# Performance work log

Hardware: AMD Instinct MI355X
Metric: run time of the kernel (lower is better)

## Reference

```python
import jax, jax.numpy as jnp
import numpy as np

WPB = [4, 2, 2]          # words_per_block per scale
NH = 8                   # num_heads
DIM = 256                # feature dim (uniform, required by cross-scale einsums)
HD = DIM // NH           # per-head feature dim
W_PAR, W_PEER, W_KID = 0.5, 1.0, 2.0


def _linear(x, W):
    # torch nn.Linear (no bias): W is [out, in]
    return jnp.einsum('bhwi,oi->bhwo', x, W)


def _split_heads(y):
    # 'b h w (k f) -> b k h w f'
    b, H, Wd, D = y.shape
    return jnp.transpose(y.reshape(b, H, Wd, NH, D // NH), (0, 3, 1, 2, 4))


def _query(x, W):
    return _split_heads(_linear(x, W))


def _kv(x, W):
    # 'b h w (i k f) -> i b k h w f' with i=2
    y = _linear(x, W)
    b, H, Wd, D = y.shape
    y = y.reshape(b, H, Wd, 2, NH, D // (2 * NH))
    y = jnp.transpose(y, (3, 0, 4, 1, 2, 5))
    return y[0], y[1]


def _blocks(x, hb):
    # 'b k (h1 h2) (w1 w2) f -> b k h1 w1 (h2 w2) f'
    b, k, H, Wd, f = x.shape
    h1, w1 = H // hb, Wd // hb
    x = x.reshape(b, k, h1, hb, w1, hb, f)
    return jnp.transpose(x, (0, 1, 2, 4, 3, 5, 6)).reshape(b, k, h1, w1, hb * hb, f)


def _forward(xs, qpeer, kvpeer, qpar, kvpar, qkid, kvkid):
    n = len(WPB)
    outs = []
    for i in range(n):
        hb = WPB[i]
        hk = WPB[i + 1] if i < n - 1 else 0
        npar = 1 if i > 0 else 0
        scale = (hb + npar + hk) ** -0.5  # coupled scaling (decouple_scales=False)
        x = xs[i]
        b, Hi, Wi, _ = x.shape
        h1, w1 = Hi // hb, Wi // hb
        L = hb * hb  # queries per block
        attn, val, wts = [], [], []
        # --- peers ---
        qp = _blocks(_query(x, qpeer[i]), hb)
        kp, vp = _kv(x, kvpeer[i])
        kp, vp = _blocks(kp, hb), _blocks(vp, hb)
        attn.append(jnp.einsum('bkhwlf,bkhwmf->bkhwlm', qp, kp) * scale)
        val.append(jnp.broadcast_to(vp[:, :, :, :, None], (b, NH, h1, w1, L, L, HD)))
        wts.append(W_PEER * jnp.ones((L,), jnp.float32))
        # --- parents ---
        if i > 0:
            qpa = _blocks(_query(x, qpar[i - 1]), hb)
            kpa, vpa = _kv(xs[i - 1], kvpar[i - 1])  # [b,k,h1,w1,f]
            attn.append(jnp.einsum('bkhwlf,bkhwf->bkhwl', qpa, kpa)[..., None] * scale)
            val.append(jnp.broadcast_to(vpa[:, :, :, :, None, None, :], (b, NH, h1, w1, L, 1, HD)))
            wts.append(W_PAR * jnp.ones((1,), jnp.float32))
        # --- kids ---
        if i < n - 1:
            g = hk * hk
            qk = _query(x, qkid[i])               # [b,k,Hi,Wi,f]
            kk, vk = _kv(xs[i + 1], kvkid[i])
            kkb = _blocks(kk, hk)                  # [b,k,Hi,Wi,g,f]
            a = jnp.einsum('bkhwf,bkhwgf->bkhwg', qk, kkb) * scale
            a = jnp.transpose(a.reshape(b, NH, h1, hb, w1, hb, g), (0, 1, 2, 4, 3, 5, 6)).reshape(b, NH, h1, w1, L, g)
            attn.append(a)
            vkb = vk.reshape(b, NH, h1, hb, hk, w1, hb, hk, HD)
            vkb = jnp.transpose(vkb, (0, 1, 2, 5, 3, 6, 4, 7, 8)).reshape(b, NH, h1, w1, L, g, HD)
            val.append(vkb)
            wts.append(W_KID * jnp.ones((g,), jnp.float32))
        V = jnp.concatenate(val, axis=-2)          # [b,k,h1,w1,L,M,f]
        wvec = jnp.concatenate(wts)                # [M]
        A = jax.nn.softmax(jnp.concatenate(attn, axis=-1), axis=-1)
        A = wvec * A
        A = A / A.sum(-1, keepdims=True)
        # NOTE: faithful to the source einsum 'bkhwlm,bkhwlnf->bkhwlf' where m and n
        # are independently summed indices (attn row-sum times value sum over n).
        o = jnp.einsum('bkhwlm,bkhwlnf->bkhwlf', A, V)
        # 'b k h1 w1 (h2 w2) f -> b (h1 h2) (w1 w2) (k f)'
        o = jnp.transpose(o.reshape(b, NH, h1, w1, hb, hb, HD), (0, 2, 4, 3, 5, 1, 6)).reshape(b, Hi, Wi, NH * HD)
        outs.append(o)
    # forward returns ms_proj_drop(ms_slf_attn): projection output is discarded in the
    # source (ms_out is overwritten), and dropout is identity at p=0.
    return tuple(outs)


def setup_inputs() -> dict:
    key = jax.random.key(0)
    ks = iter(jax.random.split(key, 24))
    B = 8
    Hs = [16, 32, 64]
    d = {}
    for i in range(3):
        d[f'x{i}'] = jax.random.normal(next(ks), (B, Hs[i], Hs[i], DIM), jnp.float32)
    for i in range(3):
        d[f'qpeer_w{i}'] = 0.02 * jax.random.normal(next(ks), (DIM, DIM), jnp.float32)
        d[f'kvpeer_w{i}'] = 0.02 * jax.random.normal(next(ks), (2 * DIM, DIM), jnp.float32)
    for i in (1, 2):
        d[f'qpar_w{i}'] = 0.02 * jax.random.normal(next(ks), (DIM, DIM), jnp.float32)
        d[f'kvpar_w{i}'] = 0.02 * jax.random.normal(next(ks), (2 * DIM, DIM), jnp.float32)
    for i in (0, 1):
        d[f'qkid_w{i}'] = 0.02 * jax.random.normal(next(ks), (DIM, DIM), jnp.float32)
        d[f'kvkid_w{i}'] = 0.02 * jax.random.normal(next(ks), (2 * DIM, DIM), jnp.float32)
    return d


def reference(x0, x1, x2, qpeer_w0, qpeer_w1, qpeer_w2, kvpeer_w0, kvpeer_w1, kvpeer_w2,
              qpar_w1, qpar_w2, kvpar_w1, kvpar_w2, qkid_w0, qkid_w1, kvkid_w0, kvkid_w1):
    return _forward([x0, x1, x2],
                    [qpeer_w0, qpeer_w1, qpeer_w2],
                    [kvpeer_w0, kvpeer_w1, kvpeer_w2],
                    [qpar_w1, qpar_w2],
                    [kvpar_w1, kvpar_w2],
                    [qkid_w0, qkid_w1],
                    [kvkid_w0, kvkid_w1])
```

## Files before the change

### kernel.cpp

```cpp
#include <hip/hip_runtime.h>


constexpr int FD = 256;

typedef __attribute__((ext_vector_type(8))) short short8;
typedef __attribute__((ext_vector_type(4))) float floatx4;

__device__ inline unsigned short bf16bits(float f) {
  unsigned u = __builtin_bit_cast(unsigned, f);
  return (unsigned short)((u + 0x7fffu + ((u >> 16) & 1u)) >> 16);
}

__device__ inline short8 load_cvt8(const float* p) {
  float4 a = *(const float4*)p;
  float4 b = *(const float4*)(p + 4);
  short8 r;
  r[0] = (short)bf16bits(a.x); r[1] = (short)bf16bits(a.y);
  r[2] = (short)bf16bits(a.z); r[3] = (short)bf16bits(a.w);
  r[4] = (short)bf16bits(b.x); r[5] = (short)bf16bits(b.y);
  r[6] = (short)bf16bits(b.z); r[7] = (short)bf16bits(b.w);
  return r;
}

constexpr size_t OFF_S1 = 144 * 256;
constexpr size_t OFF_S2 = OFF_S1 + 2048 * 256;
constexpr size_t OFF_W = OFF_S2 + 8192 * 256;

__global__ __launch_bounds__(256) void prep(
    const float4* __restrict__ x0, const float4* __restrict__ x1,
    const float4* __restrict__ x2, const float* __restrict__ wp0,
    const float* __restrict__ wk0, const float* __restrict__ wp1,
    const float* __restrict__ wq1, const float* __restrict__ wk1,
    const float* __restrict__ wp2, const float* __restrict__ wq2,
    unsigned short* __restrict__ ws) {
  int blk = blockIdx.x;
  int t = threadIdx.x;
  if (blk < 2592) {
    const float4* x;
    unsigned short* S;
    int Hs, Ws, hb, row0;
    if (blk < 32) {
      x = x0; S = ws; Hs = 4; Ws = 4; hb = 4; row0 = blk * 4;
    } else if (blk < 544) {
      x = x1; S = ws + OFF_S1; Hs = 16; Ws = 16; hb = 2; row0 = (blk - 32) * 4;
    } else {
      x = x2; S = ws + OFF_S2; Hs = 32; Ws = 32; hb = 2; row0 = (blk - 544) * 4;
    }
    int c = t & 63;
    int row = row0 + (t >> 6);
    int bw = row % Ws;
    int t2 = row / Ws;
    int bh = t2 % Hs;
    int b = t2 / Hs;
    int W = Ws * hb;
    const float4* xb =
        x + (((size_t)b * Hs * hb + bh * hb) * W + bw * hb) * 64 + c;
    float4 s = {0.f, 0.f, 0.f, 0.f};
    for (int i = 0; i < hb; ++i)
      for (int j = 0; j < hb; ++j) {
        float4 v = xb[((size_t)i * W + j) * 64];
        s.x += v.x; s.y += v.y; s.z += v.z; s.w += v.w;
      }
    ushort4 o = {bf16bits(s.x), bf16bits(s.y), bf16bits(s.z), bf16bits(s.w)};
    *(ushort4*)(S + (size_t)row * FD + c * 4) = o;
  } else {
    int wb = blk - 2592;
    int mat = wb >> 6;
    int row = (wb & 63) * 4 + (t >> 6);
    int c4 = (t & 63) * 4;
    const float* src;
    switch (mat) {
      case 0: src = wp0; break;
      case 1: src = wk0; break;
      case 2: src = wp1; break;
      case 3: src = wq1; break;
      case 4: src = wk1; break;
      case 5: src = wp2; break;
      default: src = wq2; break;
    }
    float4 v = *(const float4*)(src + (size_t)(256 + row) * FD + c4);
    ushort4 o = {bf16bits(v.x), bf16bits(v.y), bf16bits(v.z), bf16bits(v.w)};
    *(ushort4*)(ws + OFF_W + (size_t)mat * 65536 + (size_t)row * FD + c4) = o;
  }
}

#define MFMA(a, b, c) __builtin_amdgcn_mfma_f32_16x16x32_bf16(a, b, c, 0, 0, 0)

__global__ __launch_bounds__(256) void gemm12(
    const unsigned short* __restrict__ ws, const float* __restrict__ x0,
    float* __restrict__ out0, float* __restrict__ out1) {
  bool segB = blockIdx.x >= 128;
  int bid = segB ? blockIdx.x - 128 : blockIdx.x;
  int r0 = (bid >> 2) * 64;
  int n0 = (bid & 3) * 64;
  int l = threadIdx.x & 63;
  int wv = threadIdx.x >> 6;
  int c = l & 15, q = l >> 4;
  int n = n0 + wv * 16 + c;
  const short8* S1b = (const short8*)(ws + OFF_S1);
  const short8* Wb = (const short8*)(ws + OFF_W);
  const short8* aS[4];
#pragma unroll
  for (int mt = 0; mt < 4; ++mt)
    aS[mt] = S1b + (size_t)(r0 + mt * 16 + c) * 32 + q;

  if (!segB) {
    const short8* aC = (const short8*)ws + (size_t)((r0 >> 4) + c) * 32 + q;
    const short8* bK = Wb + (size_t)1 * 8192 + n * 32 + q;
    const short8* bP = Wb + (size_t)0 * 8192 + n * 32 + q;
    floatx4 accK[4] = {0, 0, 0, 0};
    floatx4 accC = {0, 0, 0, 0};
#pragma unroll 2
    for (int kk = 0; kk < 8; ++kk) {
      short8 b0 = bK[kk * 4];
      short8 b1 = bP[kk * 4];
#pragma unroll
      for (int mt = 0; mt < 4; ++mt) accK[mt] = MFMA(aS[mt][kk * 4], b0, accK[mt]);
      accC = MFMA(aC[kk * 4], b1, accC);
    }
    float s0 = __shfl(accC[0], c), s1 = __shfl(accC[1], c);
    float s2 = __shfl(accC[2], c), s3 = __shfl(accC[3], c);
    float cv = q == 0 ? s0 : q == 1 ? s1 : q == 2 ? s2 : s3;
#pragma unroll
    for (int mt = 0; mt < 4; ++mt)
#pragma unroll
      for (int r = 0; r < 4; ++r) {
        int row = r0 + mt * 16 + 4 * q + r;
        out0[(size_t)row * FD + n] = accK[mt][r] + cv;
      }
  } else {
    const float* aX[4];
#pragma unroll
    for (int mt = 0; mt < 4; ++mt)
      aX[mt] = x0 + (size_t)(r0 + mt * 16 + c) * FD + q * 8;
    const short8* bP = Wb + (size_t)2 * 8192 + n * 32 + q;
    const short8* bQ = Wb + (size_t)3 * 8192 + n * 32 + q;
    floatx4 acc[4] = {0, 0, 0, 0};
#pragma unroll 2
    for (int kk = 0; kk < 8; ++kk) {
      short8 b0 = bP[kk * 4];
      short8 b1 = bQ[kk * 4];
#pragma unroll
      for (int mt = 0; mt < 4; ++mt) {
        acc[mt] = MFMA(aS[mt][kk * 4], b0, acc[mt]);
        acc[mt] = MFMA(load_cvt8(aX[mt] + kk * 32), b1, acc[mt]);
      }
    }
#pragma unroll
    for (int mt = 0; mt < 4; ++mt)
#pragma unroll
      for (int r = 0; r < 4; ++r) {
        int rg = r0 + mt * 16 + 4 * q + r;
        int b = rg >> 8, h = (rg >> 4) & 15, w = rg & 15;
        size_t o = ((size_t)b * 1024 + h * 64 + 2 * w) * FD + n;
        float v = acc[mt][r];
        out1[o] = v;
        out1[o + FD] = v;
        out1[o + 8192] = v;
        out1[o + 8192 + FD] = v;
      }
  }
}

__global__ __launch_bounds__(256) void gemm3(
    const unsigned short* __restrict__ ws, const float* __restrict__ x1,
    float* __restrict__ out1, float* __restrict__ out2) {
  int r0 = (blockIdx.x >> 2) * 64;
  int n0 = (blockIdx.x & 3) * 64;
  int l = threadIdx.x & 63;
  int wv = threadIdx.x >> 6;
  int c = l & 15, q = l >> 4;
  int n = n0 + wv * 16 + c;
  const short8* S2b = (const short8*)(ws + OFF_S2);
  const short8* Wb = (const short8*)(ws + OFF_W);
  const short8* aS[4];
  const float* aX[4];
#pragma unroll
  for (int mt = 0; mt < 4; ++mt) {
    aS[mt] = S2b + (size_t)(r0 + mt * 16 + c) * 32 + q;
    aX[mt] = x1 + (size_t)(r0 + mt * 16 + c) * FD + q * 8;
  }
  const short8* bK = Wb + (size_t)4 * 8192 + n * 32 + q;
  const short8* bP = Wb + (size_t)5 * 8192 + n * 32 + q;
  const short8* bQ = Wb + (size_t)6 * 8192 + n * 32 + q;
  floatx4 accK[4] = {0, 0, 0, 0};
  floatx4 accC[4] = {0, 0, 0, 0};
#pragma unroll 2
  for (int kk = 0; kk < 8; ++kk) {
    short8 b0 = bK[kk * 4];
    short8 b1 = bP[kk * 4];
    short8 b2 = bQ[kk * 4];
#pragma unroll
    for (int mt = 0; mt < 4; ++mt) {
      short8 a = aS[mt][kk * 4];
      accK[mt] = MFMA(a, b0, accK[mt]);
      accC[mt] = MFMA(a, b1, accC[mt]);
      accC[mt] = MFMA(load_cvt8(aX[mt] + kk * 32), b2, accC[mt]);
    }
  }
#pragma unroll
  for (int mt = 0; mt < 4; ++mt)
#pragma unroll
    for (int r = 0; r < 4; ++r) {
      int rg = r0 + mt * 16 + 4 * q + r;
      size_t o1 = (size_t)rg * FD + n;
      out1[o1] += accK[mt][r];
      int b = rg >> 10, h = (rg >> 5) & 31, w = rg & 31;
      size_t o = ((size_t)b * 4096 + h * 128 + 2 * w) * FD + n;
      float v = accC[mt][r];
      out2[o] = v;
      out2[o + FD] = v;
      out2[o + 16384] = v;
      out2[o + 16384 + FD] = v;
    }
}

extern "C" void kernel_launch(void* const* d_in, const int* in_sizes, int n_in,
                              void* d_out, int out_size, void* d_ws,
                              size_t ws_size, hipStream_t stream) {
  const float* x0 = (const float*)d_in[0];
  const float* x1 = (const float*)d_in[1];
  const float* x2 = (const float*)d_in[2];

  const float *kvpeer0, *kvpeer1, *kvpeer2, *kvpar1, *kvpar2, *kvkid0, *kvkid1;
  if (n_in > 4 && in_sizes[4] == 2 * FD * FD) {
    kvpeer0 = (const float*)d_in[4];
    kvpeer1 = (const float*)d_in[6];
    kvpeer2 = (const float*)d_in[8];
    kvpar1 = (const float*)d_in[10];
    kvpar2 = (const float*)d_in[12];
    kvkid0 = (const float*)d_in[14];
    kvkid1 = (const float*)d_in[16];
  } else {
    kvpeer0 = (const float*)d_in[6];
    kvpeer1 = (const float*)d_in[7];
    kvpeer2 = (const float*)d_in[8];
    kvpar1 = (const float*)d_in[11];
    kvpar2 = (const float*)d_in[12];
    kvkid0 = (const float*)d_in[15];
    kvkid1 = (const float*)d_in[16];
  }

  unsigned short* ws = (unsigned short*)d_ws;
  float* out0 = (float*)d_out;
  float* out1 = out0 + (size_t)8 * 16 * 16 * FD;
  float* out2 = out1 + (size_t)8 * 32 * 32 * FD;

  prep<<<3040, 256, 0, stream>>>((const float4*)x0, (const float4*)x1,
                                 (const float4*)x2, kvpeer0, kvkid0, kvpeer1,
                                 kvpar1, kvkid1, kvpeer2, kvpar2, ws);
  gemm12<<<256, 256, 0, stream>>>(ws, x0, out0, out1);
  gemm3<<<512, 256, 0, stream>>>(ws, x1, out1, out2);
}
```

Measured before the change: 174.5 us.

## Merge gemm12 and gemm3 into one launch, pre-converting x0/x1 to bf16 in prep

The prep kernel now also writes bf16 copies of x0 and x1 to workspace while it sums blocks, so the GEMMs no longer convert fp32 activations inside their inner loops. The two GEMM kernels are merged into one 640-block launch. Each out1 tile now computes the parent contribution itself and adds it to the kid term through LDS, instead of gemm3 doing a read-modify-write of out1 after gemm12. This removes a launch, a kernel boundary and an extra out1 pass, at the cost of more workspace traffic in prep and some redundant parent-term MFMAs in each block.

```diff
diff --git a/kernel.cpp b/kernel.cpp
--- a/kernel.cpp
+++ b/kernel.cpp
@@ -10,21 +10,18 @@
   unsigned u = __builtin_bit_cast(unsigned, f);
   return (unsigned short)((u + 0x7fffu + ((u >> 16) & 1u)) >> 16);
 }
-
-__device__ inline short8 load_cvt8(const float* p) {
-  float4 a = *(const float4*)p;
-  float4 b = *(const float4*)(p + 4);
-  short8 r;
-  r[0] = (short)bf16bits(a.x); r[1] = (short)bf16bits(a.y);
-  r[2] = (short)bf16bits(a.z); r[3] = (short)bf16bits(a.w);
-  r[4] = (short)bf16bits(b.x); r[5] = (short)bf16bits(b.y);
-  r[6] = (short)bf16bits(b.z); r[7] = (short)bf16bits(b.w);
-  return r;
+__device__ inline ushort4 cvt4(float4 v) {
+  ushort4 o;
+  o.x = bf16bits(v.x); o.y = bf16bits(v.y);
+  o.z = bf16bits(v.z); o.w = bf16bits(v.w);
+  return o;
 }
 
 constexpr size_t OFF_S1 = 144 * 256;
 constexpr size_t OFF_S2 = OFF_S1 + 2048 * 256;
 constexpr size_t OFF_W = OFF_S2 + 8192 * 256;
+constexpr size_t OFF_X0 = OFF_W + 7 * 65536;
+constexpr size_t OFF_X1 = OFF_X0 + 2048 * 256;
 
 __global__ __launch_bounds__(256) void prep(
     const float4* __restrict__ x0, const float4* __restrict__ x1,
@@ -38,11 +35,13 @@
   if (blk < 2592) {
     const float4* x;
     unsigned short* S;
+    unsigned short* xo = nullptr;
     int Hs, Ws, hb, row0;
     if (blk < 32) {
-      x = x0; S = ws; Hs = 4; Ws = 4; hb = 4; row0 = blk * 4;
+      x = x0; S = ws; xo = ws + OFF_X0; Hs = 4; Ws = 4; hb = 4; row0 = blk * 4;
     } else if (blk < 544) {
-      x = x1; S = ws + OFF_S1; Hs = 16; Ws = 16; hb = 2; row0 = (blk - 32) * 4;
+      x = x1; S = ws + OFF_S1; xo = ws + OFF_X1;
+      Hs = 16; Ws = 16; hb = 2; row0 = (blk - 32) * 4;
     } else {
       x = x2; S = ws + OFF_S2; Hs = 32; Ws = 32; hb = 2; row0 = (blk - 544) * 4;
     }
@@ -53,16 +52,16 @@
     int bh = t2 % Hs;
     int b = t2 / Hs;
     int W = Ws * hb;
-    const float4* xb =
-        x + (((size_t)b * Hs * hb + bh * hb) * W + bw * hb) * 64 + c;
+    size_t base4 = (((size_t)b * Hs * hb + bh * hb) * W + bw * hb) * 64 + c;
+    const float4* xb = x + base4;
     float4 s = {0.f, 0.f, 0.f, 0.f};
     for (int i = 0; i < hb; ++i)
       for (int j = 0; j < hb; ++j) {
-        float4 v = xb[((size_t)i * W + j) * 64];
+        float4 v = xb[(size_t)(i * W + j) * 64];
         s.x += v.x; s.y += v.y; s.z += v.z; s.w += v.w;
+        if (xo) *(ushort4*)(xo + (base4 + (size_t)(i * W + j) * 64) * 4) = cvt4(v);
       }
-    ushort4 o = {bf16bits(s.x), bf16bits(s.y), bf16bits(s.z), bf16bits(s.w)};
-    *(ushort4*)(S + (size_t)row * FD + c * 4) = o;
+    *(ushort4*)(S + (size_t)row * FD + c * 4) = cvt4(s);
   } else {
     int wb = blk - 2592;
     int mat = wb >> 6;
@@ -79,44 +78,100 @@
       default: src = wq2; break;
     }
     float4 v = *(const float4*)(src + (size_t)(256 + row) * FD + c4);
-    ushort4 o = {bf16bits(v.x), bf16bits(v.y), bf16bits(v.z), bf16bits(v.w)};
-    *(ushort4*)(ws + OFF_W + (size_t)mat * 65536 + (size_t)row * FD + c4) = o;
+    *(ushort4*)(ws + OFF_W + (size_t)mat * 65536 + (size_t)row * FD + c4) =
+        cvt4(v);
   }
 }
 
 #define MFMA(a, b, c) __builtin_amdgcn_mfma_f32_16x16x32_bf16(a, b, c, 0, 0, 0)
 
-__global__ __launch_bounds__(256) void gemm12(
-    const unsigned short* __restrict__ ws, const float* __restrict__ x0,
-    float* __restrict__ out0, float* __restrict__ out1) {
-  bool segB = blockIdx.x >= 128;
-  int bid = segB ? blockIdx.x - 128 : blockIdx.x;
-  int r0 = (bid >> 2) * 64;
-  int n0 = (bid & 3) * 64;
-  int l = threadIdx.x & 63;
-  int wv = threadIdx.x >> 6;
+__global__ __launch_bounds__(256) void gemm(const unsigned short* __restrict__ ws,
+                                            float* __restrict__ out0,
+                                            float* __restrict__ out1,
+                                            float* __restrict__ out2) {
+  __shared__ float lds[4][16][17];
+  int t = threadIdx.x;
+  int l = t & 63;
+  int wv = t >> 6;
   int c = l & 15, q = l >> 4;
-  int n = n0 + wv * 16 + c;
-  const short8* S1b = (const short8*)(ws + OFF_S1);
   const short8* Wb = (const short8*)(ws + OFF_W);
-  const short8* aS[4];
-#pragma unroll
-  for (int mt = 0; mt < 4; ++mt)
-    aS[mt] = S1b + (size_t)(r0 + mt * 16 + c) * 32 + q;
-
-  if (!segB) {
+
+  if (blockIdx.x < 512) {
+    int r0 = (blockIdx.x >> 2) * 64;
+    int n0 = (blockIdx.x & 3) * 64;
+    int n = n0 + wv * 16 + c;
+    const short8* S2b = (const short8*)(ws + OFF_S2);
+    const short8* X1b = (const short8*)(ws + OFF_X1);
+    int cb0 = (r0 >> 10) * 256 + (((r0 >> 5) & 31) >> 1) * 16;
+    const short8* aS1 = (const short8*)(ws + OFF_S1) + (size_t)(cb0 + c) * 32 + q;
+    const short8* aX0 = (const short8*)(ws + OFF_X0) + (size_t)(cb0 + c) * 32 + q;
+    const short8 *aS2[4], *aX1[4];
+#pragma unroll
+    for (int mt = 0; mt < 4; ++mt) {
+      aS2[mt] = S2b + (size_t)(r0 + mt * 16 + c) * 32 + q;
+      aX1[mt] = X1b + (size_t)(r0 + mt * 16 + c) * 32 + q;
+    }
+    const short8* bK1 = Wb + (size_t)4 * 8192 + (size_t)n * 32 + q;
+    const short8* bP2 = Wb + (size_t)5 * 8192 + (size_t)n * 32 + q;
+    const short8* bQ2 = Wb + (size_t)6 * 8192 + (size_t)n * 32 + q;
+    const short8* bP1 = Wb + (size_t)2 * 8192 + (size_t)n * 32 + q;
+    const short8* bQ1 = Wb + (size_t)3 * 8192 + (size_t)n * 32 + q;
+    floatx4 accK[4] = {0, 0, 0, 0};
+    floatx4 accC2[4] = {0, 0, 0, 0};
+    floatx4 accC1 = {0, 0, 0, 0};
+#pragma unroll 2
+    for (int kk = 0; kk < 8; ++kk) {
+      short8 k1 = bK1[kk * 4], p2 = bP2[kk * 4], q2 = bQ2[kk * 4];
+      short8 p1 = bP1[kk * 4], q1 = bQ1[kk * 4];
+      accC1 = MFMA(aS1[kk * 4], p1, accC1);
+      accC1 = MFMA(aX0[kk * 4], q1, accC1);
+#pragma unroll
+      for (int mt = 0; mt < 4; ++mt) {
+        short8 a = aS2[mt][kk * 4];
+        accK[mt] = MFMA(a, k1, accK[mt]);
+        accC2[mt] = MFMA(a, p2, accC2[mt]);
+        accC2[mt] = MFMA(aX1[mt][kk * 4], q2, accC2[mt]);
+      }
+    }
+#pragma unroll
+    for (int r = 0; r < 4; ++r) lds[wv][4 * q + r][c] = accC1[r];
+    __syncthreads();
+#pragma unroll
+    for (int mt = 0; mt < 4; ++mt)
+#pragma unroll
+      for (int r = 0; r < 4; ++r) {
+        int rg = r0 + mt * 16 + 4 * q + r;
+        int w = rg & 31;
+        out1[(size_t)rg * FD + n] = accK[mt][r] + lds[wv][w >> 1][c];
+        int b = rg >> 10, h = (rg >> 5) & 31;
+        size_t o = ((size_t)b * 4096 + h * 128 + 2 * w) * FD + n;
+        float v = accC2[mt][r];
+        out2[o] = v;
+        out2[o + FD] = v;
+        out2[o + 16384] = v;
+        out2[o + 16384 + FD] = v;
+      }
+  } else {
+    int bid = blockIdx.x - 512;
+    int r0 = (bid >> 2) * 64;
+    int n0 = (bid & 3) * 64;
+    int n = n0 + wv * 16 + c;
+    const short8* S1b = (const short8*)(ws + OFF_S1);
     const short8* aC = (const short8*)ws + (size_t)((r0 >> 4) + c) * 32 + q;
-    const short8* bK = Wb + (size_t)1 * 8192 + n * 32 + q;
-    const short8* bP = Wb + (size_t)0 * 8192 + n * 32 + q;
+    const short8* bK = Wb + (size_t)1 * 8192 + (size_t)n * 32 + q;
+    const short8* bP = Wb + (size_t)0 * 8192 + (size_t)n * 32 + q;
+    const short8* aS[4];
+#pragma unroll
+    for (int mt = 0; mt < 4; ++mt)
+      aS[mt] = S1b + (size_t)(r0 + mt * 16 + c) * 32 + q;
     floatx4 accK[4] = {0, 0, 0, 0};
     floatx4 accC = {0, 0, 0, 0};
 #pragma unroll 2
     for (int kk = 0; kk < 8; ++kk) {
-      short8 b0 = bK[kk * 4];
-      short8 b1 = bP[kk * 4];
+      short8 b0 = bK[kk * 4], b1 = bP[kk * 4];
+      accC = MFMA(aC[kk * 4], b1, accC);
 #pragma unroll
       for (int mt = 0; mt < 4; ++mt) accK[mt] = MFMA(aS[mt][kk * 4], b0, accK[mt]);
-      accC = MFMA(aC[kk * 4], b1, accC);
     }
     float s0 = __shfl(accC[0], c), s1 = __shfl(accC[1], c);
     float s2 = __shfl(accC[2], c), s3 = __shfl(accC[3], c);
@@ -124,95 +179,9 @@
 #pragma unroll
     for (int mt = 0; mt < 4; ++mt)
 #pragma unroll
-      for (int r = 0; r < 4; ++r) {
-        int row = r0 + mt * 16 + 4 * q + r;
-        out0[(size_t)row * FD + n] = accK[mt][r] + cv;
-      }
-  } else {
-    const float* aX[4];
-#pragma unroll
-    for (int mt = 0; mt < 4; ++mt)
-      aX[mt] = x0 + (size_t)(r0 + mt * 16 + c) * FD + q * 8;
-    const short8* bP = Wb + (size_t)2 * 8192 + n * 32 + q;
-    const short8* bQ = Wb + (size_t)3 * 8192 + n * 32 + q;
-    floatx4 acc[4] = {0, 0, 0, 0};
-#pragma unroll 2
-    for (int kk = 0; kk < 8; ++kk) {
-      short8 b0 = bP[kk * 4];
-      short8 b1 = bQ[kk * 4];
-#pragma unroll
-      for (int mt = 0; mt < 4; ++mt) {
-        acc[mt] = MFMA(aS[mt][kk * 4], b0, acc[mt]);
-        acc[mt] = MFMA(load_cvt8(aX[mt] + kk * 32), b1, acc[mt]);
-      }
-    }
-#pragma unroll
-    for (int mt = 0; mt < 4; ++mt)
-#pragma unroll
-      for (int r = 0; r < 4; ++r) {
-        int rg = r0 + mt * 16 + 4 * q + r;
-        int b = rg >> 8, h = (rg >> 4) & 15, w = rg & 15;
-        size_t o = ((size_t)b * 1024 + h * 64 + 2 * w) * FD + n;
-        float v = acc[mt][r];
-        out1[o] = v;
-        out1[o + FD] = v;
-        out1[o + 8192] = v;
-        out1[o + 8192 + FD] = v;
-      }
+      for (int r = 0; r < 4; ++r)
+        out0[(size_t)(r0 + mt * 16 + 4 * q + r) * FD + n] = accK[mt][r] + cv;
   }
-}
-
-__global__ __launch_bounds__(256) void gemm3(
-    const unsigned short* __restrict__ ws, const float* __restrict__ x1,
-    float* __restrict__ out1, float* __restrict__ out2) {
-  int r0 = (blockIdx.x >> 2) * 64;
-  int n0 = (blockIdx.x & 3) * 64;
-  int l = threadIdx.x & 63;
-  int wv = threadIdx.x >> 6;
-  int c = l & 15, q = l >> 4;
-  int n = n0 + wv * 16 + c;
-  const short8* S2b = (const short8*)(ws + OFF_S2);
-  const short8* Wb = (const short8*)(ws + OFF_W);
-  const short8* aS[4];
-  const float* aX[4];
-#pragma unroll
-  for (int mt = 0; mt < 4; ++mt) {
-    aS[mt] = S2b + (size_t)(r0 + mt * 16 + c) * 32 + q;
-    aX[mt] = x1 + (size_t)(r0 + mt * 16 + c) * FD + q * 8;
-  }
-  const short8* bK = Wb + (size_t)4 * 8192 + n * 32 + q;
-  const short8* bP = Wb + (size_t)5 * 8192 + n * 32 + q;
-  const short8* bQ = Wb + (size_t)6 * 8192 + n * 32 + q;
-  floatx4 accK[4] = {0, 0, 0, 0};
-  floatx4 accC[4] = {0, 0, 0, 0};
-#pragma unroll 2
-  for (int kk = 0; kk < 8; ++kk) {
-    short8 b0 = bK[kk * 4];
-    short8 b1 = bP[kk * 4];
-    short8 b2 = bQ[kk * 4];
-#pragma unroll
-    for (int mt = 0; mt < 4; ++mt) {
-      short8 a = aS[mt][kk * 4];
-      accK[mt] = MFMA(a, b0, accK[mt]);
-      accC[mt] = MFMA(a, b1, accC[mt]);
-      accC[mt] = MFMA(load_cvt8(aX[mt] + kk * 32), b2, accC[mt]);
-    }
-  }
-#pragma unroll
-  for (int mt = 0; mt < 4; ++mt)
-#pragma unroll
-    for (int r = 0; r < 4; ++r) {
-      int rg = r0 + mt * 16 + 4 * q + r;
-      size_t o1 = (size_t)rg * FD + n;
-      out1[o1] += accK[mt][r];
-      int b = rg >> 10, h = (rg >> 5) & 31, w = rg & 31;
-      size_t o = ((size_t)b * 4096 + h * 128 + 2 * w) * FD + n;
-      float v = accC[mt][r];
-      out2[o] = v;
-      out2[o + FD] = v;
-      out2[o + 16384] = v;
-      out2[o + 16384 + FD] = v;
-    }
 }
 
 extern "C" void kernel_launch(void* const* d_in, const int* in_sizes, int n_in,
@@ -249,6 +218,5 @@
   prep<<<3040, 256, 0, stream>>>((const float4*)x0, (const float4*)x1,
                                  (const float4*)x2, kvpeer0, kvkid0, kvpeer1,
                                  kvpar1, kvkid1, kvpeer2, kvpar2, ws);
-  gemm12<<<256, 256, 0, stream>>>(ws, x0, out0, out1);
-  gemm3<<<512, 256, 0, stream>>>(ws, x1, out1, out2);
-}
+  gemm<<<640, 256, 0, stream>>>(ws, out0, out1, out2);
+}
```

After: 167.7 us. 1.04x faster.
